# Performance work log

Hardware: AMD Instinct MI355X
Metric: run time of the kernel (lower is better)

The kernel has to match this reference:

```python
import jax, jax.numpy as jnp
import numpy as np

D = 1024      # model dim (used for theta exponent and 1/sqrt(d) scale)
D_H = 128     # head dim


def make_theta():
    # theta[i] = 10 ** (-2*(i-1)/d), each value repeated twice -> length d_H
    i = np.repeat(np.arange(D_H // 2), 2)
    return jnp.asarray(10.0 ** (-2.0 * (i - 1) / D), dtype=jnp.float32)


def rotation(x, theta):
    # x: [B, T, d_H]; positions are 1..T (source uses arange(1, T+1))
    B, T, dh = x.shape
    idx = jnp.arange(1, T + 1, dtype=x.dtype)[:, None]          # [T, 1]
    ang = idx * theta[None, :]                                   # [T, d_H]
    cos, sin = jnp.cos(ang), jnp.sin(ang)
    # pairwise swap with sign: (x0, x1) -> (x1, -x0)
    x2 = x.reshape(B, T, dh // 2, 2)
    swapped = jnp.stack([x2[..., 1], -x2[..., 0]], axis=-1).reshape(B, T, dh)
    return x * cos + swapped * sin


def setup_inputs() -> dict:
    key = jax.random.key(0)
    kx, kq, kk, kv = jax.random.split(key, 4)
    B, T = 4, 2048
    scale = 1.0 / np.sqrt(D)
    return {
        "x": jax.random.normal(kx, (B, T, D), dtype=jnp.float32),
        "Wq": jax.random.normal(kq, (D_H, D), dtype=jnp.float32) * scale,
        "Wk": jax.random.normal(kk, (D_H, D), dtype=jnp.float32) * scale,
        "Wv": jax.random.normal(kv, (D_H, D), dtype=jnp.float32) * scale,
        "theta": make_theta(),
    }


def reference(x, Wq, Wk, Wv, theta):
    B, T, d = x.shape
    Q = jnp.einsum('btd,hd->bth', x, Wq)
    K = jnp.einsum('btd,hd->bth', x, Wk)
    V = jnp.einsum('btd,hd->bth', x, Wv)
    Q = rotation(Q, theta)
    K = rotation(K, theta)
    # scale uses model dim d (not d_H), as in the source
    scores = jnp.einsum('bqh,bkh->bqk', Q, K) * (d ** -0.5)
    causal = jnp.tril(jnp.ones((T, T), dtype=bool))
    scores = jnp.where(causal, scores, -jnp.inf)
    attn = jax.nn.softmax(scores, axis=-1)
    return jnp.einsum('bqk,bkh->bqh', attn, V)
```

## Files before the change

kernel.cpp:

```cpp
#include <hip/hip_runtime.h>
#include <math.h>

#define T_SEQ 2048
#define D_MODEL 1024
#define DH 128
#define SLOTS 288
#define FRAG_B 262144

typedef __bf16 bfx8 __attribute__((ext_vector_type(8)));
typedef float f32x4 __attribute__((ext_vector_type(4)));

union U16x8 { uint4 u4; unsigned int ui[4]; unsigned short us[8]; __bf16 bf[8]; bfx8 v; };

__device__ inline uint4 cvt8u(float4 a, float4 b) {
    U16x8 u;
    u.bf[0] = (__bf16)a.x; u.bf[1] = (__bf16)a.y; u.bf[2] = (__bf16)a.z; u.bf[3] = (__bf16)a.w;
    u.bf[4] = (__bf16)b.x; u.bf[5] = (__bf16)b.y; u.bf[6] = (__bf16)b.z; u.bf[7] = (__bf16)b.w;
    return u.u4;
}

__device__ inline bfx8 cvt8v(float4 a, float4 b) {
    U16x8 u;
    u.bf[0] = (__bf16)a.x; u.bf[1] = (__bf16)a.y; u.bf[2] = (__bf16)a.z; u.bf[3] = (__bf16)a.w;
    u.bf[4] = (__bf16)b.x; u.bf[5] = (__bf16)b.y; u.bf[6] = (__bf16)b.z; u.bf[7] = (__bf16)b.w;
    return u.v;
}

__device__ inline int slot_base32(int qt) {
    int g = qt >> 3, j = qt & 7;
    return 4 * g * (g + 1) + j * (g + 1);
}

__global__ __launch_bounds__(256) void prep_w_kernel(
    const float* __restrict__ Wq, const float* __restrict__ Wk,
    const float* __restrict__ Wv, __bf16* __restrict__ WF)
{
    const int i = blockIdx.x * 256 + threadIdx.x;
    const int wsel = i >> 14;
    const int i2 = i & 16383;
    const int kc = i2 >> 9, j = (i2 >> 6) & 7, ln = i2 & 63;
    const int lo = ln & 15, quad = ln >> 4;
    const float* src = (wsel == 0) ? Wq : (wsel == 1) ? Wk : Wv;
    const float* p = src + (size_t)(j * 16 + lo) * D_MODEL + kc * 32 + quad * 8;
    float4 a = *(const float4*)p;
    float4 b = *(const float4*)(p + 4);
    *(uint4*)&WF[(size_t)((wsel * 32 + kc) * 8 + j) * 512 + ln * 8] = cvt8u(a, b);
}

__global__ __launch_bounds__(64) void qkv_kernel(
    const float* __restrict__ x, const __bf16* __restrict__ WF,
    const float* __restrict__ theta,
    __bf16* __restrict__ QF, __bf16* __restrict__ KF, __bf16* __restrict__ VF)
{
    __shared__ __align__(16) unsigned short T[32 * 136];

    const int bx = blockIdx.x;
    const int wsel = bx >> 8;
    const int m0 = (bx & 255) * 32;

    const int ln = threadIdx.x;
    const int lo = ln & 15, quad = ln >> 4;

    const __bf16* WFp = WF + (size_t)wsel * (32 * 8 * 512);
    const float* xr0 = x + (size_t)(m0 + lo) * D_MODEL + quad * 8;
    const float* xr1 = xr0 + (size_t)16 * D_MODEL;

    float4 xA[2][2], xB[2][2];
    bfx8 wA[8], wB[8];

    xA[0][0] = *(const float4*)(xr0);      xA[0][1] = *(const float4*)(xr0 + 4);
    xA[1][0] = *(const float4*)(xr1);      xA[1][1] = *(const float4*)(xr1 + 4);
    xB[0][0] = *(const float4*)(xr0 + 32); xB[0][1] = *(const float4*)(xr0 + 36);
    xB[1][0] = *(const float4*)(xr1 + 32); xB[1][1] = *(const float4*)(xr1 + 36);
    #pragma unroll
    for (int j = 0; j < 8; ++j) {
        wA[j] = *(const bfx8*)&WFp[(size_t)j * 512 + ln * 8];
        wB[j] = *(const bfx8*)&WFp[(size_t)(8 + j) * 512 + ln * 8];
    }

    f32x4 acc[2][8];
    #pragma unroll
    for (int iq = 0; iq < 2; ++iq)
        #pragma unroll
        for (int j = 0; j < 8; ++j) acc[iq][j] = (f32x4)(0.f);

    for (int kc = 0; kc < 32; kc += 2) {
        {
            const int kp = (kc + 2 < 32) ? (kc + 2) : kc;
            bfx8 x0 = cvt8v(xA[0][0], xA[0][1]);
            bfx8 x1 = cvt8v(xA[1][0], xA[1][1]);
            xA[0][0] = *(const float4*)(xr0 + kp * 32);
            xA[0][1] = *(const float4*)(xr0 + kp * 32 + 4);
            xA[1][0] = *(const float4*)(xr1 + kp * 32);
            xA[1][1] = *(const float4*)(xr1 + kp * 32 + 4);
            #pragma unroll
            for (int j = 0; j < 8; ++j) {
                acc[0][j] = __builtin_amdgcn_mfma_f32_16x16x32_bf16(x0, wA[j], acc[0][j], 0, 0, 0);
                acc[1][j] = __builtin_amdgcn_mfma_f32_16x16x32_bf16(x1, wA[j], acc[1][j], 0, 0, 0);
                wA[j] = *(const bfx8*)&WFp[(size_t)(kp * 8 + j) * 512 + ln * 8];
            }
        }
        {
            const int kp = (kc + 3 < 32) ? (kc + 3) : (kc + 1);
            bfx8 x0 = cvt8v(xB[0][0], xB[0][1]);
            bfx8 x1 = cvt8v(xB[1][0], xB[1][1]);
            xB[0][0] = *(const float4*)(xr0 + kp * 32);
            xB[0][1] = *(const float4*)(xr0 + kp * 32 + 4);
            xB[1][0] = *(const float4*)(xr1 + kp * 32);
            xB[1][1] = *(const float4*)(xr1 + kp * 32 + 4);
            #pragma unroll
            for (int j = 0; j < 8; ++j) {
                acc[0][j] = __builtin_amdgcn_mfma_f32_16x16x32_bf16(x0, wB[j], acc[0][j], 0, 0, 0);
                acc[1][j] = __builtin_amdgcn_mfma_f32_16x16x32_bf16(x1, wB[j], acc[1][j], 0, 0, 0);
                wB[j] = *(const bfx8*)&WFp[(size_t)(kp * 8 + j) * 512 + ln * 8];
            }
        }
    }

    const int b = m0 >> 11;
    const int mloc0 = m0 & (T_SEQ - 1);

    if (wsel < 2) {
        __bf16* dstP = (wsel == 0 ? QF : KF) + (size_t)b * FRAG_B;
        const int t16l = mloc0 >> 4;
        #pragma unroll
        for (int iq = 0; iq < 2; ++iq) {
            #pragma unroll
            for (int j = 0; j < 8; ++j) {
                const int h = j * 16 + lo;
                const float th = theta[h];
                #pragma unroll
                for (int r = 0; r < 4; ++r) {
                    const int pos = mloc0 + iq * 16 + quad * 4 + r + 1;
                    float v = acc[iq][j][r];
                    float partner = __shfl_xor(v, 1, 64);
                    float ang = (float)pos * th;
                    float rev = ang * 0.15915494309189535f;
                    rev -= floorf(rev);
                    float sn = __builtin_amdgcn_sinf(rev);
                    float cs = __builtin_amdgcn_cosf(rev);
                    float res = (h & 1) ? (v * cs - partner * sn)
                                        : (v * cs + partner * sn);
                    U16x8 u; u.bf[0] = (__bf16)res;
                    T[(quad * 4 + r) * 136 + h] = u.us[0];
                }
            }
            #pragma unroll
            for (int c4 = 0; c4 < 4; ++c4) {
                uint4 d = *(const uint4*)&T[(ln & 15) * 136 + c4 * 32 + (ln >> 4) * 8];
                *(uint4*)&dstP[(size_t)((t16l + iq) * 4 + c4) * 512 + ln * 8] = d;
            }
        }
    } else {
        const int kt32 = mloc0 >> 5;
        #pragma unroll
        for (int iq = 0; iq < 2; ++iq)
            #pragma unroll
            for (int j = 0; j < 8; ++j)
                #pragma unroll
                for (int r = 0; r < 4; ++r) {
                    U16x8 u; u.bf[0] = (__bf16)acc[iq][j][r];
                    T[(iq * 16 + quad * 4 + r) * 136 + j * 16 + lo] = u.us[0];
                }
        __bf16* dstP = VF + (size_t)b * FRAG_B;
        #pragma unroll
        for (int j = 0; j < 8; ++j) {
            U16x8 u;
            #pragma unroll
            for (int e = 0; e < 8; ++e)
                u.us[e] = T[((ln >> 4) * 8 + e) * 136 + j * 16 + (ln & 15)];
            *(uint4*)&dstP[(size_t)(kt32 * 8 + j) * 512 + ln * 8] = u.u4;
        }
    }
}

__global__ __launch_bounds__(64) void attn_partial_kernel(
    const __bf16* __restrict__ QF, const __bf16* __restrict__ KF,
    const __bf16* __restrict__ VF,
    __bf16* __restrict__ Opb, float* __restrict__ Ll)
{
    const int qt = blockIdx.x, c = blockIdx.y, b = blockIdx.z;
    const int qbase = qt * 32;
    const int kstart = c << 8;
    if (kstart > qbase) return;
    const int nt = min(8, (qbase + 32 - kstart) >> 5);

    __shared__ __align__(16) unsigned short Pw[2 * 640];

    const int ln = threadIdx.x;
    const int lo = ln & 15, quad = ln >> 4;
    const int hi8 = quad * 8;

    const __bf16* QFb = QF + (size_t)b * FRAG_B;
    const __bf16* KFb = KF + (size_t)b * FRAG_B;
    const __bf16* VFb = VF + (size_t)b * FRAG_B;

    bfx8 qf[2][4];
    #pragma unroll
    for (int iq = 0; iq < 2; ++iq)
        #pragma unroll
        for (int c4 = 0; c4 < 4; ++c4)
            qf[iq][c4] = *(const bfx8*)&QFb[(size_t)((qt * 2 + iq) * 4 + c4) * 512 + ln * 8];

    f32x4 O[2][8];
    #pragma unroll
    for (int iq = 0; iq < 2; ++iq)
        #pragma unroll
        for (int j = 0; j < 8; ++j) O[iq][j] = (f32x4)(0.f);
    float lsum[2][4];
    #pragma unroll
    for (int iq = 0; iq < 2; ++iq)
        #pragma unroll
        for (int r = 0; r < 4; ++r) lsum[iq][r] = 0.f;

    bfx8 kcur[2][4], knxt[2][4];
    #pragma unroll
    for (int jj = 0; jj < 2; ++jj)
        #pragma unroll
        for (int c4 = 0; c4 < 4; ++c4)
            kcur[jj][c4] = *(const bfx8*)&KFb[(size_t)(((kstart >> 4) + jj) * 4 + c4) * 512 + ln * 8];

    for (int kt = 0; kt < nt; ++kt) {
        const int k0 = kstart + kt * 32;
        bfx8 vf[8];
        #pragma unroll
        for (int j = 0; j < 8; ++j)
            vf[j] = *(const bfx8*)&VFb[(size_t)((k0 >> 5) * 8 + j) * 512 + ln * 8];
        if (kt + 1 < nt) {
            const int kn16 = (k0 + 32) >> 4;
            #pragma unroll
            for (int jj = 0; jj < 2; ++jj)
                #pragma unroll
                for (int c4 = 0; c4 < 4; ++c4)
                    knxt[jj][c4] = *(const bfx8*)&KFb[(size_t)((kn16 + jj) * 4 + c4) * 512 + ln * 8];
        }

        f32x4 s4[2][2];
        #pragma unroll
        for (int iq = 0; iq < 2; ++iq)
            #pragma unroll
            for (int jj = 0; jj < 2; ++jj) s4[iq][jj] = (f32x4)(0.f);
        #pragma unroll
        for (int c4 = 0; c4 < 4; ++c4)
            #pragma unroll
            for (int iq = 0; iq < 2; ++iq)
                #pragma unroll
                for (int jj = 0; jj < 2; ++jj)
                    s4[iq][jj] = __builtin_amdgcn_mfma_f32_16x16x32_bf16(qf[iq][c4], kcur[jj][c4], s4[iq][jj], 0, 0, 0);

        const bool needMask = (k0 + 31 > qbase);
        #pragma unroll
        for (int iq = 0; iq < 2; ++iq)
            #pragma unroll
            for (int jj = 0; jj < 2; ++jj)
                #pragma unroll
                for (int r = 0; r < 4; ++r) {
                    const int col = k0 + jj * 16 + lo;
                    const int row = qbase + iq * 16 + quad * 4 + r;
                    float p = __expf(s4[iq][jj][r] * 0.03125f);
                    if (needMask && col > row) p = 0.f;
                    lsum[iq][r] += p;
                    U16x8 u; u.bf[0] = (__bf16)p;
                    Pw[iq * 640 + (quad * 4 + r) * 40 + jj * 16 + lo] = u.us[0];
                }

        bfx8 pf0 = *(const bfx8*)&Pw[lo * 40 + hi8];
        bfx8 pf1 = *(const bfx8*)&Pw[640 + lo * 40 + hi8];
        #pragma unroll
        for (int j = 0; j < 8; ++j) {
            O[0][j] = __builtin_amdgcn_mfma_f32_16x16x32_bf16(pf0, vf[j], O[0][j], 0, 0, 0);
            O[1][j] = __builtin_amdgcn_mfma_f32_16x16x32_bf16(pf1, vf[j], O[1][j], 0, 0, 0);
        }

        #pragma unroll
        for (int jj = 0; jj < 2; ++jj)
            #pragma unroll
            for (int c4 = 0; c4 < 4; ++c4) kcur[jj][c4] = knxt[jj][c4];
    }

    #pragma unroll
    for (int off = 1; off < 16; off <<= 1)
        #pragma unroll
        for (int iq = 0; iq < 2; ++iq)
            #pragma unroll
            for (int r = 0; r < 4; ++r) lsum[iq][r] += __shfl_xor(lsum[iq][r], off, 64);

    const size_t sb = (size_t)b * SLOTS + slot_base32(qt) + c;
    #pragma unroll
    for (int iq = 0; iq < 2; ++iq)
        #pragma unroll
        for (int j = 0; j < 8; ++j) {
            U16x8 u;
            u.bf[0] = (__bf16)O[iq][j][0]; u.bf[1] = (__bf16)O[iq][j][1];
            u.bf[2] = (__bf16)O[iq][j][2]; u.bf[3] = (__bf16)O[iq][j][3];
            *(uint2*)&Opb[((sb * 2 + iq) * 8 + j) * 256 + ln * 4] = make_uint2(u.ui[0], u.ui[1]);
        }
    if (lo == 0) {
        #pragma unroll
        for (int iq = 0; iq < 2; ++iq)
            #pragma unroll
            for (int r = 0; r < 4; ++r)
                Ll[sb * 32 + iq * 16 + quad * 4 + r] = lsum[iq][r];
    }
}

__global__ __launch_bounds__(128) void attn_merge_kernel(
    const __bf16* __restrict__ Opb, const float* __restrict__ Ll,
    float* __restrict__ out)
{
    const int qt = blockIdx.x, b = blockIdx.y, j = blockIdx.z;
    const int g = qt >> 3, nc = g + 1;
    const size_t base = (size_t)b * SLOTS + slot_base32(qt);

    __shared__ float Lsh[8][32];
    const int tid = threadIdx.x;
    const int iq = tid >> 6, ln = tid & 63;
    const int lo = ln & 15, quad = ln >> 4;

    for (int idx = tid; idx < nc * 32; idx += 128)
        Lsh[idx >> 5][idx & 31] = Ll[(base + (idx >> 5)) * 32 + (idx & 31)];
    __syncthreads();

    float acc[4] = {0.f, 0.f, 0.f, 0.f};
    for (int cc = 0; cc < nc; ++cc) {
        uint2 d = *(const uint2*)&Opb[(((base + cc) * 2 + iq) * 8 + j) * 256 + ln * 4];
        U16x8 u; u.ui[0] = d.x; u.ui[1] = d.y;
        #pragma unroll
        for (int r = 0; r < 4; ++r) acc[r] += (float)u.bf[r];
    }

    #pragma unroll
    for (int r = 0; r < 4; ++r) {
        const int row = iq * 16 + quad * 4 + r;
        float l = 0.f;
        for (int cc = 0; cc < nc; ++cc) l += Lsh[cc][row];
        out[((size_t)b * T_SEQ + qt * 32 + row) * DH + j * 16 + lo] = acc[r] / l;
    }
}

extern "C" void kernel_launch(void* const* d_in, const int* in_sizes, int n_in,
                              void* d_out, int out_size, void* d_ws, size_t ws_size,
                              hipStream_t stream) {
    const float* x     = (const float*)d_in[0];
    const float* Wq    = (const float*)d_in[1];
    const float* Wk    = (const float*)d_in[2];
    const float* Wv    = (const float*)d_in[3];
    const float* theta = (const float*)d_in[4];
    float* out = (float*)d_out;

    const int M = in_sizes[0] / D_MODEL;
    const int B = M / T_SEQ;

    __bf16* WF  = (__bf16*)d_ws;
    __bf16* QF  = WF + (size_t)3 * 32 * 8 * 512;
    __bf16* KF  = QF + (size_t)B * FRAG_B;
    __bf16* VF  = KF + (size_t)B * FRAG_B;
    __bf16* Opb = VF + (size_t)B * FRAG_B;
    float*  Ll  = (float*)(Opb + (size_t)B * SLOTS * 2 * 8 * 256);

    prep_w_kernel<<<dim3(192), 256, 0, stream>>>(Wq, Wk, Wv, WF);
    qkv_kernel<<<dim3(3 * (M / 32)), 64, 0, stream>>>(x, WF, theta, QF, KF, VF);
    attn_partial_kernel<<<dim3(T_SEQ / 32, 8, B), 64, 0, stream>>>(QF, KF, VF, Opb, Ll);
    attn_merge_kernel<<<dim3(T_SEQ / 32, B, 8), 128, 0, stream>>>(Opb, Ll, out);
}
```

Baseline: 143.0 us.

## Split QKV projection across four waves with split-K and LDS reduction

The QKV projection block grows from one wave to four. Each wave handles half of the K dimension and half of the output head columns. The two K-halves are combined through a shared-memory float buffer, and then the rotary epilogue and stores are spread across all four waves. This is meant to cut the per-block serial MFMA chain and give more parallelism and latency hiding for the 768 blocks. The cost is extra LDS traffic, more barriers, and redundant x loads, since both jh waves read the same x.

```diff
diff --git a/kernel.cpp b/kernel.cpp
--- a/kernel.cpp
+++ b/kernel.cpp
@@ -47,46 +47,52 @@
     *(uint4*)&WF[(size_t)((wsel * 32 + kc) * 8 + j) * 512 + ln * 8] = cvt8u(a, b);
 }
 
-__global__ __launch_bounds__(64) void qkv_kernel(
+__global__ __launch_bounds__(256, 4) void qkv_kernel(
     const float* __restrict__ x, const __bf16* __restrict__ WF,
     const float* __restrict__ theta,
     __bf16* __restrict__ QF, __bf16* __restrict__ KF, __bf16* __restrict__ VF)
 {
+    __shared__ float R[2 * 8 * 4 * 64];
     __shared__ __align__(16) unsigned short T[32 * 136];
 
     const int bx = blockIdx.x;
     const int wsel = bx >> 8;
     const int m0 = (bx & 255) * 32;
 
-    const int ln = threadIdx.x;
+    const int tid = threadIdx.x;
+    const int ln = tid & 63;
+    const int w  = tid >> 6;
+    const int kh = w >> 1;
+    const int jh = w & 1;
     const int lo = ln & 15, quad = ln >> 4;
 
-    const __bf16* WFp = WF + (size_t)wsel * (32 * 8 * 512);
+    const __bf16* WFp = WF + (size_t)wsel * (32 * 8 * 512) + (size_t)jh * 4 * 512;
     const float* xr0 = x + (size_t)(m0 + lo) * D_MODEL + quad * 8;
     const float* xr1 = xr0 + (size_t)16 * D_MODEL;
+    const int kc0 = kh * 16, kcE = kc0 + 16;
 
     float4 xA[2][2], xB[2][2];
-    bfx8 wA[8], wB[8];
-
-    xA[0][0] = *(const float4*)(xr0);      xA[0][1] = *(const float4*)(xr0 + 4);
-    xA[1][0] = *(const float4*)(xr1);      xA[1][1] = *(const float4*)(xr1 + 4);
-    xB[0][0] = *(const float4*)(xr0 + 32); xB[0][1] = *(const float4*)(xr0 + 36);
-    xB[1][0] = *(const float4*)(xr1 + 32); xB[1][1] = *(const float4*)(xr1 + 36);
-    #pragma unroll
-    for (int j = 0; j < 8; ++j) {
-        wA[j] = *(const bfx8*)&WFp[(size_t)j * 512 + ln * 8];
-        wB[j] = *(const bfx8*)&WFp[(size_t)(8 + j) * 512 + ln * 8];
-    }
-
-    f32x4 acc[2][8];
+    bfx8 wA[4], wB[4];
+
+    xA[0][0] = *(const float4*)(xr0 + kc0 * 32);      xA[0][1] = *(const float4*)(xr0 + kc0 * 32 + 4);
+    xA[1][0] = *(const float4*)(xr1 + kc0 * 32);      xA[1][1] = *(const float4*)(xr1 + kc0 * 32 + 4);
+    xB[0][0] = *(const float4*)(xr0 + kc0 * 32 + 32); xB[0][1] = *(const float4*)(xr0 + kc0 * 32 + 36);
+    xB[1][0] = *(const float4*)(xr1 + kc0 * 32 + 32); xB[1][1] = *(const float4*)(xr1 + kc0 * 32 + 36);
+    #pragma unroll
+    for (int jl = 0; jl < 4; ++jl) {
+        wA[jl] = *(const bfx8*)&WFp[((size_t)kc0 * 8 + jl) * 512 + ln * 8];
+        wB[jl] = *(const bfx8*)&WFp[((size_t)(kc0 + 1) * 8 + jl) * 512 + ln * 8];
+    }
+
+    f32x4 acc[2][4];
     #pragma unroll
     for (int iq = 0; iq < 2; ++iq)
         #pragma unroll
-        for (int j = 0; j < 8; ++j) acc[iq][j] = (f32x4)(0.f);
-
-    for (int kc = 0; kc < 32; kc += 2) {
+        for (int jl = 0; jl < 4; ++jl) acc[iq][jl] = (f32x4)(0.f);
+
+    for (int kc = kc0; kc < kcE; kc += 2) {
         {
-            const int kp = (kc + 2 < 32) ? (kc + 2) : kc;
+            const int kp = (kc + 2 < kcE) ? kc + 2 : kc;
             bfx8 x0 = cvt8v(xA[0][0], xA[0][1]);
             bfx8 x1 = cvt8v(xA[1][0], xA[1][1]);
             xA[0][0] = *(const float4*)(xr0 + kp * 32);
@@ -94,14 +100,14 @@
             xA[1][0] = *(const float4*)(xr1 + kp * 32);
             xA[1][1] = *(const float4*)(xr1 + kp * 32 + 4);
             #pragma unroll
-            for (int j = 0; j < 8; ++j) {
-                acc[0][j] = __builtin_amdgcn_mfma_f32_16x16x32_bf16(x0, wA[j], acc[0][j], 0, 0, 0);
-                acc[1][j] = __builtin_amdgcn_mfma_f32_16x16x32_bf16(x1, wA[j], acc[1][j], 0, 0, 0);
-                wA[j] = *(const bfx8*)&WFp[(size_t)(kp * 8 + j) * 512 + ln * 8];
+            for (int jl = 0; jl < 4; ++jl) {
+                acc[0][jl] = __builtin_amdgcn_mfma_f32_16x16x32_bf16(x0, wA[jl], acc[0][jl], 0, 0, 0);
+                acc[1][jl] = __builtin_amdgcn_mfma_f32_16x16x32_bf16(x1, wA[jl], acc[1][jl], 0, 0, 0);
+                wA[jl] = *(const bfx8*)&WFp[((size_t)kp * 8 + jl) * 512 + ln * 8];
             }
         }
         {
-            const int kp = (kc + 3 < 32) ? (kc + 3) : (kc + 1);
+            const int kp = (kc + 3 < kcE) ? kc + 3 : kc + 1;
             bfx8 x0 = cvt8v(xB[0][0], xB[0][1]);
             bfx8 x1 = cvt8v(xB[1][0], xB[1][1]);
             xB[0][0] = *(const float4*)(xr0 + kp * 32);
@@ -109,13 +115,36 @@
             xB[1][0] = *(const float4*)(xr1 + kp * 32);
             xB[1][1] = *(const float4*)(xr1 + kp * 32 + 4);
             #pragma unroll
-            for (int j = 0; j < 8; ++j) {
-                acc[0][j] = __builtin_amdgcn_mfma_f32_16x16x32_bf16(x0, wB[j], acc[0][j], 0, 0, 0);
-                acc[1][j] = __builtin_amdgcn_mfma_f32_16x16x32_bf16(x1, wB[j], acc[1][j], 0, 0, 0);
-                wB[j] = *(const bfx8*)&WFp[(size_t)(kp * 8 + j) * 512 + ln * 8];
+            for (int jl = 0; jl < 4; ++jl) {
+                acc[0][jl] = __builtin_amdgcn_mfma_f32_16x16x32_bf16(x0, wB[jl], acc[0][jl], 0, 0, 0);
+                acc[1][jl] = __builtin_amdgcn_mfma_f32_16x16x32_bf16(x1, wB[jl], acc[1][jl], 0, 0, 0);
+                wB[jl] = *(const bfx8*)&WFp[((size_t)kp * 8 + jl) * 512 + ln * 8];
             }
         }
     }
+
+    if (kh == 1) {
+        #pragma unroll
+        for (int iq = 0; iq < 2; ++iq)
+            #pragma unroll
+            for (int jl = 0; jl < 4; ++jl)
+                #pragma unroll
+                for (int r = 0; r < 4; ++r)
+                    R[((iq * 8 + jh * 4 + jl) * 4 + r) * 64 + ln] = acc[iq][jl][r];
+    }
+    __syncthreads();
+    if (kh == 0) {
+        #pragma unroll
+        for (int iq = 0; iq < 2; ++iq)
+            #pragma unroll
+            for (int jl = 0; jl < 4; ++jl)
+                #pragma unroll
+                for (int r = 0; r < 4; ++r) {
+                    const int idx = ((iq * 8 + jh * 4 + jl) * 4 + r) * 64 + ln;
+                    R[idx] += acc[iq][jl][r];
+                }
+    }
+    __syncthreads();
 
     const int b = m0 >> 11;
     const int mloc0 = m0 & (T_SEQ - 1);
@@ -126,13 +155,14 @@
         #pragma unroll
         for (int iq = 0; iq < 2; ++iq) {
             #pragma unroll
-            for (int j = 0; j < 8; ++j) {
+            for (int jl2 = 0; jl2 < 2; ++jl2) {
+                const int j = 2 * w + jl2;
                 const int h = j * 16 + lo;
                 const float th = theta[h];
                 #pragma unroll
                 for (int r = 0; r < 4; ++r) {
                     const int pos = mloc0 + iq * 16 + quad * 4 + r + 1;
-                    float v = acc[iq][j][r];
+                    float v = R[((iq * 8 + j) * 4 + r) * 64 + ln];
                     float partner = __shfl_xor(v, 1, 64);
                     float ang = (float)pos * th;
                     float rev = ang * 0.15915494309189535f;
@@ -142,29 +172,34 @@
                     float res = (h & 1) ? (v * cs - partner * sn)
                                         : (v * cs + partner * sn);
                     U16x8 u; u.bf[0] = (__bf16)res;
-                    T[(quad * 4 + r) * 136 + h] = u.us[0];
+                    T[(iq * 16 + quad * 4 + r) * 136 + h] = u.us[0];
                 }
             }
-            #pragma unroll
-            for (int c4 = 0; c4 < 4; ++c4) {
-                uint4 d = *(const uint4*)&T[(ln & 15) * 136 + c4 * 32 + (ln >> 4) * 8];
-                *(uint4*)&dstP[(size_t)((t16l + iq) * 4 + c4) * 512 + ln * 8] = d;
-            }
+        }
+        __syncthreads();
+        #pragma unroll
+        for (int iq = 0; iq < 2; ++iq) {
+            uint4 d = *(const uint4*)&T[(iq * 16 + (ln & 15)) * 136 + w * 32 + (ln >> 4) * 8];
+            *(uint4*)&dstP[(size_t)((t16l + iq) * 4 + w) * 512 + ln * 8] = d;
         }
     } else {
-        const int kt32 = mloc0 >> 5;
-        #pragma unroll
-        for (int iq = 0; iq < 2; ++iq)
-            #pragma unroll
-            for (int j = 0; j < 8; ++j)
+        #pragma unroll
+        for (int iq = 0; iq < 2; ++iq)
+            #pragma unroll
+            for (int jl2 = 0; jl2 < 2; ++jl2) {
+                const int j = 2 * w + jl2;
                 #pragma unroll
                 for (int r = 0; r < 4; ++r) {
-                    U16x8 u; u.bf[0] = (__bf16)acc[iq][j][r];
+                    U16x8 u; u.bf[0] = (__bf16)R[((iq * 8 + j) * 4 + r) * 64 + ln];
                     T[(iq * 16 + quad * 4 + r) * 136 + j * 16 + lo] = u.us[0];
                 }
+            }
+        __syncthreads();
         __bf16* dstP = VF + (size_t)b * FRAG_B;
-        #pragma unroll
-        for (int j = 0; j < 8; ++j) {
+        const int kt32 = mloc0 >> 5;
+        #pragma unroll
+        for (int jl2 = 0; jl2 < 2; ++jl2) {
+            const int j = 2 * w + jl2;
             U16x8 u;
             #pragma unroll
             for (int e = 0; e < 8; ++e)
@@ -359,7 +394,7 @@
     float*  Ll  = (float*)(Opb + (size_t)B * SLOTS * 2 * 8 * 256);
 
     prep_w_kernel<<<dim3(192), 256, 0, stream>>>(Wq, Wk, Wv, WF);
-    qkv_kernel<<<dim3(3 * (M / 32)), 64, 0, stream>>>(x, WF, theta, QF, KF, VF);
+    qkv_kernel<<<dim3(3 * (M / 32)), 256, 0, stream>>>(x, WF, theta, QF, KF, VF);
     attn_partial_kernel<<<dim3(T_SEQ / 32, 8, B), 64, 0, stream>>>(QF, KF, VF, Opb, Ll);
     attn_merge_kernel<<<dim3(T_SEQ / 32, B, 8), 128, 0, stream>>>(Opb, Ll, out);
 }
```

Result: slower. 166.0 us (+16.1%).
